# Kernel tuning notes

Hardware: AMD Instinct MI355X
Metric: run time of the kernel (lower is better)

## Reference

```python
import jax, jax.numpy as jnp
import numpy as np

CH = 512
NUM_HEADS = 8
NUM_GROUPS = 32  # min(32, channels)
EPS = 1e-5


def setup_inputs() -> dict:
    key = jax.random.key(0)
    ks = jax.random.split(key, 4)
    B, C, H, W = 8, CH, 32, 32
    x = jax.random.normal(ks[0], (B, C, H, W), dtype=jnp.float32)
    gn_weight = jnp.ones((C,), dtype=jnp.float32)
    gn_bias = jnp.zeros((C,), dtype=jnp.float32)
    # 1x1 conv weights stored as [out_ch, in_ch] (kernel dims squeezed)
    qkv_weight = jax.random.normal(ks[1], (3 * C, C), dtype=jnp.float32) * (C ** -0.5)
    qkv_bias = jnp.zeros((3 * C,), dtype=jnp.float32)
    proj_weight = jax.random.normal(ks[2], (C, C), dtype=jnp.float32) * (C ** -0.5)
    proj_bias = jnp.zeros((C,), dtype=jnp.float32)
    return {
        "x": x,
        "gn_weight": gn_weight,
        "gn_bias": gn_bias,
        "qkv_weight": qkv_weight,
        "qkv_bias": qkv_bias,
        "proj_weight": proj_weight,
        "proj_bias": proj_bias,
    }


def _group_norm(x, weight, bias):
    B, C, H, W = x.shape
    g = x.reshape(B, NUM_GROUPS, C // NUM_GROUPS, H, W)
    mean = jnp.mean(g, axis=(2, 3, 4), keepdims=True)
    var = jnp.var(g, axis=(2, 3, 4), keepdims=True)
    g = (g - mean) * jax.lax.rsqrt(var + EPS)
    g = g.reshape(B, C, H, W)
    return g * weight[None, :, None, None] + bias[None, :, None, None]


def reference(x, gn_weight, gn_bias, qkv_weight, qkv_bias, proj_weight, proj_bias):
    B, C, H, W = x.shape
    nh = NUM_HEADS
    hc = C // nh
    N = H * W

    h = _group_norm(x, gn_weight, gn_bias)
    # 1x1 conv == per-pixel matmul
    qkv = jnp.einsum('oc,bchw->bohw', qkv_weight, h) + qkv_bias[None, :, None, None]
    q, k, v = jnp.split(qkv, 3, axis=1)
    # b (h c) x y -> b h c (x y)
    q = q.reshape(B, nh, hc, N)
    k = k.reshape(B, nh, hc, N)
    v = v.reshape(B, nh, hc, N)

    scale = hc ** -0.5
    attn = jnp.einsum('bhci,bhcj->bhij', q, k) * scale  # [B, nh, N, N]
    attn = jax.nn.softmax(attn, axis=-1)
    out = jnp.einsum('bhij,bhcj->bhci', attn, v)  # [B, nh, hc, N]
    out = out.reshape(B, C, H, W)
    out = jnp.einsum('oc,bchw->bohw', proj_weight, out) + proj_bias[None, :, None, None]
    return x + out
```

## Files before the change

kernel.cpp:

```cpp
#include <hip/hip_runtime.h>
#include <math.h>

#define B_   8
#define C_   512
#define N_   1024
#define NH_  8
#define HC_  64

typedef __attribute__((ext_vector_type(8))) short bf16x8;
typedef __attribute__((ext_vector_type(4))) float f32x4;

#define MFMA16(a, b, c) __builtin_amdgcn_mfma_f32_16x16x32_bf16(a, b, c, 0, 0, 0)

__device__ __forceinline__ unsigned short f2bf(float f) {
  unsigned u = __builtin_bit_cast(unsigned, f);
  u += 0x7fffu + ((u >> 16) & 1u);
  return (unsigned short)(u >> 16);
}

__device__ __forceinline__ unsigned short f2bf_trunc(float f) {
  return (unsigned short)(__builtin_bit_cast(unsigned, f) >> 16);
}

__device__ __forceinline__ unsigned pack2(float a, float b) {
  return (unsigned)f2bf(a) | ((unsigned)f2bf(b) << 16);
}

__device__ __forceinline__ void gll16(const void* g, void* l) {
  __builtin_amdgcn_global_load_lds(
      (const __attribute__((address_space(1))) unsigned int*)g,
      (__attribute__((address_space(3))) unsigned int*)l, 16, 0, 0);
}

__global__ __launch_bounds__(256) void prep(const float* __restrict__ x,
                                            const float* __restrict__ gw,
                                            const float* __restrict__ gb,
                                            const float* __restrict__ qkvw,
                                            const float* __restrict__ pw,
                                            unsigned short* __restrict__ hT,
                                            unsigned short* __restrict__ qkvw_bf,
                                            unsigned short* __restrict__ projw_bf) {
  const int t = threadIdx.x;
  if (blockIdx.x >= 256) {
    const int widx = blockIdx.x - 256;
    const float* src = (widx < 768) ? qkvw : pw;
    unsigned short* dst = (widx < 768) ? qkvw_bf : projw_bf;
    const int i = ((widx < 768) ? widx : widx - 768) * 1024 + t * 4;
    const float4 v = *(const float4*)(src + i);
    ushort4 o;
    o.x = f2bf(v.x); o.y = f2bf(v.y); o.z = f2bf(v.z); o.w = f2bf(v.w);
    *(ushort4*)(dst + i) = o;
    return;
  }
  const int b = blockIdx.x >> 5;
  const int g = blockIdx.x & 31;
  const float* xg = x + ((size_t)b * C_ + (size_t)g * 16) * N_;

  float4 xv[16];
  float s = 0.f, ss = 0.f;
#pragma unroll
  for (int k = 0; k < 16; ++k) {
    xv[k] = *(const float4*)(xg + (size_t)k * N_ + t * 4);
    s  += xv[k].x + xv[k].y + xv[k].z + xv[k].w;
    ss += xv[k].x * xv[k].x + xv[k].y * xv[k].y + xv[k].z * xv[k].z + xv[k].w * xv[k].w;
  }
#pragma unroll
  for (int off = 32; off > 0; off >>= 1) {
    s  += __shfl_down(s, off);
    ss += __shfl_down(ss, off);
  }
  __shared__ float rs[4], rss[4], sh_mi[2];
  if ((t & 63) == 0) { rs[t >> 6] = s; rss[t >> 6] = ss; }
  __syncthreads();
  if (t == 0) {
    s  = rs[0] + rs[1] + rs[2] + rs[3];
    ss = rss[0] + rss[1] + rss[2] + rss[3];
    const float mean = s * (1.f / 16384.f);
    const float var  = ss * (1.f / 16384.f) - mean * mean;
    sh_mi[0] = mean;
    sh_mi[1] = rsqrtf(var + 1e-5f);
  }
  __syncthreads();
  const float mean = sh_mi[0], inv = sh_mi[1];

  float sc[16], of[16];
#pragma unroll
  for (int k = 0; k < 16; ++k) {
    const int c = g * 16 + k;
    sc[k] = inv * gw[c];
    of[k] = gb[c] - mean * sc[k];
  }
#pragma unroll
  for (int r = 0; r < 4; ++r) {
    const int p = t * 4 + r;
    unsigned short* dst = hT + ((size_t)b * N_ + p) * C_ + g * 16;
    uint4 o0, o1;
#pragma unroll
    for (int k2 = 0; k2 < 4; ++k2) {
      const float a0 = ((const float*)&xv[k2 * 2 + 0])[r] * sc[k2 * 2 + 0] + of[k2 * 2 + 0];
      const float a1 = ((const float*)&xv[k2 * 2 + 1])[r] * sc[k2 * 2 + 1] + of[k2 * 2 + 1];
      ((unsigned*)&o0)[k2] = pack2(a0, a1);
      const float b0 = ((const float*)&xv[8 + k2 * 2 + 0])[r] * sc[8 + k2 * 2 + 0] + of[8 + k2 * 2 + 0];
      const float b1 = ((const float*)&xv[8 + k2 * 2 + 1])[r] * sc[8 + k2 * 2 + 1] + of[8 + k2 * 2 + 1];
      ((unsigned*)&o1)[k2] = pack2(b0, b1);
    }
    *(uint4*)(dst)     = o0;
    *(uint4*)(dst + 8) = o1;
  }
}

__global__ __launch_bounds__(256, 3) void gemm_qkv(
    const unsigned short* __restrict__ A, const float* __restrict__ bias,
    const unsigned short* __restrict__ BT, unsigned short* __restrict__ qkTout,
    unsigned short* __restrict__ vout) {
  __shared__ __attribute__((aligned(16))) short lds[128 * 136];
  const int t = threadIdx.x;
  const int lane = t & 63, w = t >> 6;
  const int lm = lane & 15, q = lane >> 4;
  const int wm = w >> 1, wn = w & 1;
  const int b = blockIdx.z;
  const int m0 = blockIdx.y * 128, n0 = blockIdx.x * 128;
  const unsigned short* Bb = BT + (size_t)b * N_ * C_;

  f32x4 acc[4][4];
#pragma unroll
  for (int i = 0; i < 4; ++i)
#pragma unroll
    for (int j = 0; j < 4; ++j) acc[i][j] = (f32x4){0.f, 0.f, 0.f, 0.f};

  for (int k0 = 0; k0 < C_; k0 += 64) {
    __syncthreads();
#pragma unroll
    for (int rr = 0; rr < 2; ++rr) {
      const int rg = w * 2 + rr;
#pragma unroll
      for (int ks = 0; ks < 2; ++ks) {
        gll16(A  + (size_t)(m0 + rg * 16 + lm) * C_ + k0 + ks * 32 + q * 8,
              lds + (rg * 2 + ks) * 512);
        gll16(Bb + (size_t)(n0 + rg * 16 + lm) * C_ + k0 + ks * 32 + q * 8,
              lds + (16 + rg * 2 + ks) * 512);
      }
    }
    __syncthreads();
    bf16x8 af[4][2];
#pragma unroll
    for (int mi = 0; mi < 4; ++mi)
#pragma unroll
      for (int ks = 0; ks < 2; ++ks)
        af[mi][ks] = *(const bf16x8*)(lds + (((wm * 4 + mi) * 2) + ks) * 512 + lane * 8);
#pragma unroll
    for (int ni = 0; ni < 4; ++ni)
#pragma unroll
      for (int ks = 0; ks < 2; ++ks) {
        const bf16x8 bfr =
            *(const bf16x8*)(lds + (16 + ((wn * 4 + ni) * 2) + ks) * 512 + lane * 8);
#pragma unroll
        for (int mi = 0; mi < 4; ++mi)
          acc[mi][ni] = MFMA16(af[mi][ks], bfr, acc[mi][ni]);
      }
  }

  __syncthreads();
  if (blockIdx.y < 8) {
    const float qs = (blockIdx.y < 4) ? 0.125f : 1.0f;
#pragma unroll
    for (int mi = 0; mi < 4; ++mi) {
#pragma unroll
      for (int ni = 0; ni < 4; ++ni) {
        const int pl = wn * 64 + ni * 16 + lm;
        const int ol0 = wm * 64 + mi * 16 + q * 4;
        ushort4 o4;
        o4.x = f2bf((acc[mi][ni][0] + bias[m0 + ol0 + 0]) * qs);
        o4.y = f2bf((acc[mi][ni][1] + bias[m0 + ol0 + 1]) * qs);
        o4.z = f2bf((acc[mi][ni][2] + bias[m0 + ol0 + 2]) * qs);
        o4.w = f2bf((acc[mi][ni][3] + bias[m0 + ol0 + 3]) * qs);
        *(ushort4*)&lds[pl * 136 + ol0] = o4;
      }
    }
    __syncthreads();
#pragma unroll
    for (int u = 0; u < 8; ++u) {
      const int flat = u * 256 + t;
      const int oc = flat & 15, pl = flat >> 4;
      *(uint4*)&qkTout[((size_t)b * N_ + n0 + pl) * 1024 + m0 + oc * 8] =
          *(const uint4*)&lds[pl * 136 + oc * 8];
    }
  } else {
#pragma unroll
    for (int mi = 0; mi < 4; ++mi)
#pragma unroll
      for (int ni = 0; ni < 4; ++ni) {
        const int pl = wn * 64 + ni * 16 + lm;
#pragma unroll
        for (int r = 0; r < 4; ++r) {
          const int ol = wm * 64 + mi * 16 + q * 4 + r;
          lds[ol * 136 + pl] = f2bf(acc[mi][ni][r] + bias[m0 + ol]);
        }
      }
    __syncthreads();
    const int c0 = m0 - 1024;
#pragma unroll
    for (int u = 0; u < 8; ++u) {
      const int flat = u * 256 + t;
      const int pc = flat & 15, ol = flat >> 4;
      *(uint4*)&vout[((size_t)b * 512 + c0 + ol) * N_ + n0 + pc * 8] =
          *(const uint4*)&lds[ol * 136 + pc * 8];
    }
  }
}

__global__ __launch_bounds__(256, 4) void gemm_proj(
    const unsigned short* __restrict__ A, const float* __restrict__ bias,
    const unsigned short* __restrict__ BT, const float* __restrict__ resid,
    float* __restrict__ outf) {
  __shared__ __attribute__((aligned(16))) short lds[32 * 512];
  const int t = threadIdx.x;
  const int lane = t & 63, w = t >> 6;
  const int lm = lane & 15, q = lane >> 4;
  const int wm = w >> 1, wn = w & 1;
  const int b = blockIdx.z;
  const int m0 = blockIdx.y * 64, n0 = blockIdx.x * 64;
  const unsigned short* Bb = BT + (size_t)b * N_ * C_;

  f32x4 acc[2][2];
#pragma unroll
  for (int i = 0; i < 2; ++i)
#pragma unroll
    for (int j = 0; j < 2; ++j) acc[i][j] = (f32x4){0.f, 0.f, 0.f, 0.f};

  for (int k0 = 0; k0 < C_; k0 += 128) {
    __syncthreads();
#pragma unroll
    for (int ks = 0; ks < 4; ++ks) {
      gll16(A  + (size_t)(m0 + w * 16 + lm) * C_ + k0 + ks * 32 + q * 8,
            lds + (w * 4 + ks) * 512);
      gll16(Bb + (size_t)(n0 + w * 16 + lm) * C_ + k0 + ks * 32 + q * 8,
            lds + (16 + w * 4 + ks) * 512);
    }
    __syncthreads();
#pragma unroll
    for (int ks = 0; ks < 4; ++ks) {
      bf16x8 af[2];
#pragma unroll
      for (int mi = 0; mi < 2; ++mi)
        af[mi] = *(const bf16x8*)(lds + ((wm * 2 + mi) * 4 + ks) * 512 + lane * 8);
#pragma unroll
      for (int ni = 0; ni < 2; ++ni) {
        const bf16x8 bfr =
            *(const bf16x8*)(lds + (16 + (wn * 2 + ni) * 4 + ks) * 512 + lane * 8);
#pragma unroll
        for (int mi = 0; mi < 2; ++mi)
          acc[mi][ni] = MFMA16(af[mi], bfr, acc[mi][ni]);
      }
    }
  }

#pragma unroll
  for (int mi = 0; mi < 2; ++mi)
#pragma unroll
    for (int ni = 0; ni < 2; ++ni) {
      const int col = n0 + wn * 32 + ni * 16 + lm;
#pragma unroll
      for (int r = 0; r < 4; ++r) {
        const int row = m0 + wm * 32 + mi * 16 + q * 4 + r;
        const size_t oi = ((size_t)b * 512 + row) * N_ + col;
        outf[oi] = acc[mi][ni][r] + bias[row] + resid[oi];
      }
    }
}

__global__ __launch_bounds__(256, 6) void attn_mfma(
    const unsigned short* __restrict__ qkT, const unsigned short* __restrict__ vbuf,
    unsigned short* __restrict__ aoT) {
  __shared__ __attribute__((aligned(16))) short lds[24 * 512];
  short* Ks = lds;
  short* Vs = lds + 8 * 512;
  short* Pb = lds + 16 * 512;

  const int t = threadIdx.x;
  const int lane = t & 63, w = t >> 6;
  const int lm = lane & 15, q = lane >> 4;
  const int id = blockIdx.x;
  const int xcd = id & 7, slot = id >> 3;
  const int pair = xcd * 8 + (slot >> 4);
  const int b = pair >> 3, hh = pair & 7;
  const int i0 = (slot & 15) * 64;

  const unsigned short* QT = qkT + (size_t)b * N_ * 1024;
  const unsigned short* Vp = vbuf + ((size_t)b * 512 + hh * 64) * N_;

  bf16x8 af[2];
#pragma unroll
  for (int ks = 0; ks < 2; ++ks)
    af[ks] = *(const bf16x8*)(QT + (size_t)(i0 + w * 16 + lm) * 1024 +
                              hh * 64 + ks * 32 + q * 8);

  f32x4 accO[4], lrun = (f32x4){0.f, 0.f, 0.f, 0.f};
#pragma unroll
  for (int nc = 0; nc < 4; ++nc) accO[nc] = (f32x4){0.f, 0.f, 0.f, 0.f};

  for (int jt = 0; jt < 16; ++jt) {
    const int j0 = jt * 64;
    __syncthreads();
#pragma unroll
    for (int ks = 0; ks < 2; ++ks) {
      gll16(QT + (size_t)(j0 + w * 16 + lm) * 1024 + 512 + hh * 64 + ks * 32 + q * 8,
            Ks + (w * 2 + ks) * 512);
      gll16(Vp + (size_t)(w * 16 + lm) * N_ + j0 + ks * 32 + q * 8,
            Vs + (w * 2 + ks) * 512);
    }
    __syncthreads();

    f32x4 accS[4];
#pragma unroll
    for (int nj = 0; nj < 4; ++nj) accS[nj] = (f32x4){0.f, 0.f, 0.f, 0.f};
#pragma unroll
    for (int nj = 0; nj < 4; ++nj)
#pragma unroll
      for (int ks = 0; ks < 2; ++ks) {
        const bf16x8 bfr = *(const bf16x8*)(Ks + (nj * 2 + ks) * 512 + lane * 8);
        accS[nj] = MFMA16(af[ks], bfr, accS[nj]);
      }

#pragma unroll
    for (int nj = 0; nj < 4; ++nj)
#pragma unroll
      for (int r = 0; r < 4; ++r) {
        const float p = __expf(accS[nj][r]);
        accS[nj][r] = p;
        lrun[r] += p;
      }
#pragma unroll
    for (int nj = 0; nj < 4; ++nj) {
      const int jin = nj * 16 + lm;
      const int ks = jin >> 5;
      const int qt = (jin >> 3) & 3;
      const int jp = jin & 7;
      short* pp = Pb + (w * 2 + ks) * 512 + qt * 128 + jp;
#pragma unroll
      for (int r = 0; r < 4; ++r)
        pp[(q * 4 + r) * 8] = (short)f2bf_trunc(accS[nj][r]);
    }

#pragma unroll
    for (int ks = 0; ks < 2; ++ks) {
      const bf16x8 pf = *(const bf16x8*)(Pb + (w * 2 + ks) * 512 + lane * 8);
#pragma unroll
      for (int nc = 0; nc < 4; ++nc) {
        const bf16x8 vf = *(const bf16x8*)(Vs + (nc * 2 + ks) * 512 + lane * 8);
        accO[nc] = MFMA16(pf, vf, accO[nc]);
      }
    }
  }

#pragma unroll
  for (int d = 1; d <= 8; d <<= 1)
#pragma unroll
    for (int r = 0; r < 4; ++r) lrun[r] += __shfl_xor(lrun[r], d);
  f32x4 linv;
#pragma unroll
  for (int r = 0; r < 4; ++r) linv[r] = 1.f / lrun[r];

  __syncthreads();
  short* Ep = lds + w * 1152;
#pragma unroll
  for (int nc = 0; nc < 4; ++nc)
#pragma unroll
    for (int r = 0; r < 4; ++r)
      Ep[(q * 4 + r) * 72 + nc * 16 + lm] = f2bf(accO[nc][r] * linv[r]);
  unsigned short* aob = aoT + (size_t)b * N_ * C_;
#pragma unroll
  for (int u = 0; u < 2; ++u) {
    const int flat = u * 64 + lane;
    const int c8 = flat & 7, i = flat >> 3;
    *(uint4*)&aob[(size_t)(i0 + w * 16 + i) * C_ + hh * 64 + c8 * 8] =
        *(const uint4*)&Ep[i * 72 + c8 * 8];
  }
}

extern "C" void kernel_launch(void* const* d_in, const int* in_sizes, int n_in,
                              void* d_out, int out_size, void* d_ws, size_t ws_size,
                              hipStream_t stream) {
  const float* x    = (const float*)d_in[0];
  const float* gw   = (const float*)d_in[1];
  const float* gb   = (const float*)d_in[2];
  const float* qkvw = (const float*)d_in[3];
  const float* qkvb = (const float*)d_in[4];
  const float* pw   = (const float*)d_in[5];
  const float* pb   = (const float*)d_in[6];
  float* out = (float*)d_out;

  unsigned short* hT       = (unsigned short*)d_ws;
  unsigned short* qkvw_bf  = hT + (size_t)B_ * N_ * C_;
  unsigned short* projw_bf = qkvw_bf + 1536 * 512;
  unsigned short* qkT      = projw_bf + 512 * 512;
  unsigned short* vbuf     = qkT + (size_t)B_ * N_ * 1024;
  unsigned short* aoTp     = vbuf + (size_t)B_ * 512 * N_;

  prep<<<1280, 256, 0, stream>>>(x, gw, gb, qkvw, pw, hT, qkvw_bf, projw_bf);
  gemm_qkv<<<dim3(8, 12, B_), 256, 0, stream>>>(qkvw_bf, qkvb, hT, qkT, vbuf);
  attn_mfma<<<1024, 256, 0, stream>>>(qkT, vbuf, aoTp);
  gemm_proj<<<dim3(16, 8, B_), 256, 0, stream>>>(projw_bf, pb, aoTp, x, out);
}
```

Measured before the change: 166.7 us.

## Double-buffer QKV GEMM LDS staging and pad attention P tile

The QKV projection GEMM now uses two LDS buffers with a K step of 32. The next tile is loaded asynchronously while MFMAs run on the current one, which needs only one barrier per iteration instead of two. In the attention kernel, the P staging buffer becomes a per-wave padded row-major tile with stride 72 to reduce LDS bank conflicts, and it is reused for the epilogue so the final block barrier can go. The trade-off is more GEMM iterations with less work each and a slightly larger attention LDS footprint, which could affect occupancy.

Measured after the change: 165.4 us, median of 2. No clear change (-0.7%).

```diff
diff --git a/kernel.cpp b/kernel.cpp
--- a/kernel.cpp
+++ b/kernel.cpp
@@ -128,37 +128,42 @@
 #pragma unroll
     for (int j = 0; j < 4; ++j) acc[i][j] = (f32x4){0.f, 0.f, 0.f, 0.f};
 
-  for (int k0 = 0; k0 < C_; k0 += 64) {
-    __syncthreads();
-#pragma unroll
-    for (int rr = 0; rr < 2; ++rr) {
-      const int rg = w * 2 + rr;
-#pragma unroll
-      for (int ks = 0; ks < 2; ++ks) {
-        gll16(A  + (size_t)(m0 + rg * 16 + lm) * C_ + k0 + ks * 32 + q * 8,
-              lds + (rg * 2 + ks) * 512);
-        gll16(Bb + (size_t)(n0 + rg * 16 + lm) * C_ + k0 + ks * 32 + q * 8,
-              lds + (16 + rg * 2 + ks) * 512);
-      }
-    }
-    __syncthreads();
-    bf16x8 af[4][2];
-#pragma unroll
-    for (int mi = 0; mi < 4; ++mi)
-#pragma unroll
-      for (int ks = 0; ks < 2; ++ks)
-        af[mi][ks] = *(const bf16x8*)(lds + (((wm * 4 + mi) * 2) + ks) * 512 + lane * 8);
-#pragma unroll
-    for (int ni = 0; ni < 4; ++ni)
-#pragma unroll
-      for (int ks = 0; ks < 2; ++ks) {
-        const bf16x8 bfr =
-            *(const bf16x8*)(lds + (16 + ((wn * 4 + ni) * 2) + ks) * 512 + lane * 8);
-#pragma unroll
-        for (int mi = 0; mi < 4; ++mi)
-          acc[mi][ni] = MFMA16(af[mi][ks], bfr, acc[mi][ni]);
-      }
-  }
+#define QKV_STAGE(k0, base_)                                                   \
+  {                                                                            \
+    _Pragma("unroll") for (int rr = 0; rr < 2; ++rr) {                         \
+      const int rg = w * 2 + rr;                                               \
+      gll16(A  + (size_t)(m0 + rg * 16 + lm) * C_ + (k0) + q * 8,              \
+            (base_) + rg * 512);                                               \
+      gll16(Bb + (size_t)(n0 + rg * 16 + lm) * C_ + (k0) + q * 8,              \
+            (base_) + (8 + rg) * 512);                                         \
+    }                                                                          \
+  }
+
+#define QKV_COMPUTE(base_)                                                     \
+  {                                                                            \
+    bf16x8 af[4];                                                              \
+    _Pragma("unroll") for (int mi = 0; mi < 4; ++mi)                           \
+      af[mi] = *(const bf16x8*)((base_) + (wm * 4 + mi) * 512 + lane * 8);     \
+    _Pragma("unroll") for (int ni = 0; ni < 4; ++ni) {                         \
+      const bf16x8 bfr =                                                       \
+          *(const bf16x8*)((base_) + (8 + wn * 4 + ni) * 512 + lane * 8);      \
+      _Pragma("unroll") for (int mi = 0; mi < 4; ++mi)                         \
+        acc[mi][ni] = MFMA16(af[mi], bfr, acc[mi][ni]);                        \
+    }                                                                          \
+  }
+
+  QKV_STAGE(0, lds)
+  for (int it = 0; it < 15; ++it) {
+    __syncthreads();
+    short* nxt = lds + ((it + 1) & 1) * 8192;
+    QKV_STAGE((it + 1) * 32, nxt)
+    const short* cur = lds + (it & 1) * 8192;
+    QKV_COMPUTE(cur)
+  }
+  __syncthreads();
+  QKV_COMPUTE(lds + 8192)
+#undef QKV_STAGE
+#undef QKV_COMPUTE
 
   __syncthreads();
   if (blockIdx.y < 8) {
@@ -272,7 +277,7 @@
 __global__ __launch_bounds__(256, 6) void attn_mfma(
     const unsigned short* __restrict__ qkT, const unsigned short* __restrict__ vbuf,
     unsigned short* __restrict__ aoT) {
-  __shared__ __attribute__((aligned(16))) short lds[24 * 512];
+  __shared__ __attribute__((aligned(16))) short lds[12800];
   short* Ks = lds;
   short* Vs = lds + 8 * 512;
   short* Pb = lds + 16 * 512;
@@ -288,6 +293,7 @@
 
   const unsigned short* QT = qkT + (size_t)b * N_ * 1024;
   const unsigned short* Vp = vbuf + ((size_t)b * 512 + hh * 64) * N_;
+  short* Pw = Pb + w * 1152;
 
   bf16x8 af[2];
 #pragma unroll
@@ -331,20 +337,14 @@
         lrun[r] += p;
       }
 #pragma unroll
-    for (int nj = 0; nj < 4; ++nj) {
-      const int jin = nj * 16 + lm;
-      const int ks = jin >> 5;
-      const int qt = (jin >> 3) & 3;
-      const int jp = jin & 7;
-      short* pp = Pb + (w * 2 + ks) * 512 + qt * 128 + jp;
+    for (int nj = 0; nj < 4; ++nj)
 #pragma unroll
       for (int r = 0; r < 4; ++r)
-        pp[(q * 4 + r) * 8] = (short)f2bf_trunc(accS[nj][r]);
-    }
+        Pw[(q * 4 + r) * 72 + nj * 16 + lm] = (short)f2bf_trunc(accS[nj][r]);
 
 #pragma unroll
     for (int ks = 0; ks < 2; ++ks) {
-      const bf16x8 pf = *(const bf16x8*)(Pb + (w * 2 + ks) * 512 + lane * 8);
+      const bf16x8 pf = *(const bf16x8*)(Pw + lm * 72 + ks * 32 + q * 8);
 #pragma unroll
       for (int nc = 0; nc < 4; ++nc) {
         const bf16x8 vf = *(const bf16x8*)(Vs + (nc * 2 + ks) * 512 + lane * 8);
@@ -361,20 +361,18 @@
 #pragma unroll
   for (int r = 0; r < 4; ++r) linv[r] = 1.f / lrun[r];
 
-  __syncthreads();
-  short* Ep = lds + w * 1152;
 #pragma unroll
   for (int nc = 0; nc < 4; ++nc)
 #pragma unroll
     for (int r = 0; r < 4; ++r)
-      Ep[(q * 4 + r) * 72 + nc * 16 + lm] = f2bf(accO[nc][r] * linv[r]);
+      Pw[(q * 4 + r) * 72 + nc * 16 + lm] = f2bf(accO[nc][r] * linv[r]);
   unsigned short* aob = aoT + (size_t)b * N_ * C_;
 #pragma unroll
   for (int u = 0; u < 2; ++u) {
     const int flat = u * 64 + lane;
     const int c8 = flat & 7, i = flat >> 3;
     *(uint4*)&aob[(size_t)(i0 + w * 16 + i) * C_ + hh * 64 + c8 * 8] =
-        *(const uint4*)&Ep[i * 72 + c8 * 8];
+        *(const uint4*)&Pw[i * 72 + c8 * 8];
   }
 }
 
```
